# Kernel optimization log

Hardware: AMD Instinct MI355X
Metric: run time of the kernel (lower is better)

The kernel has to match this reference:

```python
import jax, jax.numpy as jnp
import numpy as np

N_NODES = 1111
BRANCH = 10


def _build_parents(n, b):
    parents = np.zeros(n, dtype=np.int32)
    for i in range(1, n):
        parents[i] = (i - 1) // b
    return parents


def _levels_from_parents(parents):
    n = parents.shape[0]
    depth = np.zeros(n, dtype=np.int32)
    for i in range(1, n):
        depth[i] = depth[parents[i]] + 1
    return [np.nonzero(depth == d)[0] for d in range(int(depth.max()) + 1)]


def setup_inputs() -> dict:
    key = jax.random.key(0)
    ks = jax.random.split(key, 8)
    N, B, Din, M = N_NODES, 128, 300, 256
    s = 0.05
    parents = _build_parents(N, BRANCH)
    return {
        "inputs": jax.random.normal(ks[0], (N, B, Din), jnp.float32),
        "prob": jax.random.uniform(ks[1], (N, N), jnp.float32),
        "Wioux": jax.random.normal(ks[2], (3 * M, Din), jnp.float32) * s,
        "bioux": jnp.zeros((3 * M,), jnp.float32),
        "Wiouh": jax.random.normal(ks[3], (3 * M, M), jnp.float32) * s,
        "biouh": jnp.zeros((3 * M,), jnp.float32),
        "Wfx": jax.random.normal(ks[4], (M, Din), jnp.float32) * s,
        "bfx": jnp.zeros((M,), jnp.float32),
        "Wfh": jax.random.normal(ks[5], (M, M), jnp.float32) * s,
        "bfh": jnp.zeros((M,), jnp.float32),
        "parents": jnp.asarray(parents),
    }


def reference(inputs, prob, Wioux, bioux, Wiouh, biouh, Wfx, bfx, Wfh, bfh, parents):
    # inputs: [N, B, Din]; prob: [N, N]; Linear weights in torch layout [out, in].
    N, B, _ = inputs.shape
    M = Wfx.shape[0]
    parents_np = np.asarray(parents)
    levels = _levels_from_parents(parents_np)  # static tree structure

    # Input-dependent pre-activations for all nodes at once (batched over the tree).
    xiou = jnp.einsum('nbd,kd->nbk', inputs, Wioux) + bioux  # [N, B, 3M]
    xf = jnp.einsum('nbd,md->nbm', inputs, Wfx) + bfx        # [N, B, M]

    h = jnp.zeros((N, B, M), inputs.dtype)
    c = jnp.zeros((N, B, M), inputs.dtype)

    # Level-synchronous top-down pass: all nodes at a given depth share no
    # dependencies, so each level is one batched gating step (loop over ~4 levels).
    for d, idx in enumerate(levels):
        if d == 0:
            ph = jnp.zeros((len(idx), B, M), inputs.dtype)
            pc = ph
        else:
            p = parents_np[idx]
            scale = prob[p, idx][:, None, None]  # edge weight prob[parent, child]
            ph = scale * h[p]
            pc = scale * c[p]
        iou = xiou[idx] + jnp.einsum('nbm,km->nbk', ph, Wiouh) + biouh
        i, o, u = jnp.split(iou, 3, axis=-1)
        f = jax.nn.sigmoid(jnp.einsum('nbm,km->nbk', ph, Wfh) + bfh + xf[idx])
        cn = jax.nn.sigmoid(i) * jnp.tanh(u) + f * pc
        hn = jax.nn.sigmoid(o) * jnp.tanh(cn)
        c = c.at[idx].set(cn)
        h = h.at[idx].set(hn)

    # Per-node top_down_state for the whole tree (original stores these on nodes
    # and returns the root's (c, h)).
    return c, h
```

## Files before the change

kernel.cpp:

```cpp
#include <hip/hip_runtime.h>
#include <hip/hip_bf16.h>


#define NNODES 1111
#define BATCH  128
#define MDIM   256
#define DIN    300
#define NBM    (NNODES * BATCH * MDIM)
#define NCK_X  10
#define NCK_H  8
#define CHUNK_ELEMS 8192
#define XW_ELEMS (4 * NCK_X * CHUNK_ELEMS)
#define HW_ELEMS (4 * NCK_H * CHUNK_ELEMS)

typedef __attribute__((ext_vector_type(8))) short s16x8;
typedef __attribute__((ext_vector_type(4))) float f32x4;

__device__ __forceinline__ ushort f2bf(float f) {
    union { float f; unsigned u; } v; v.f = f;
    unsigned u = v.u;
    return (ushort)((u + 0x7FFFu + ((u >> 16) & 1u)) >> 16);
}
__device__ __forceinline__ float bf2f(ushort u) {
    union { unsigned u; float f; } v; v.u = ((unsigned)u) << 16;
    return v.f;
}
__device__ __forceinline__ float sigmoidf_(float x) { return 1.0f / (1.0f + __expf(-x)); }

__device__ __forceinline__ int swz(int a) { return a ^ (((a >> 6) & 7) << 4); }

__global__ void prep_kernel(
    const float* __restrict__ Wioux, const float* __restrict__ bioux,
    const float* __restrict__ Wiouh, const float* __restrict__ biouh,
    const float* __restrict__ Wfx,   const float* __restrict__ bfx,
    const float* __restrict__ Wfh,   const float* __restrict__ bfh,
    ushort* __restrict__ packWx, ushort* __restrict__ packWh,
    float* __restrict__ bias)
{
    const int idx = blockIdx.x * 256 + threadIdx.x;
    if (idx < XW_ELEMS + HW_ELEMS) {
        const bool isX = idx < XW_ELEMS;
        const int id   = isX ? idx : idx - XW_ELEMS;
        const int nck  = isX ? NCK_X : NCK_H;
        const int strip = id / (nck * CHUNK_ELEMS);
        const int rem   = id % (nck * CHUNK_ELEMS);
        const int ck    = rem / CHUNK_ELEMS;
        const int e     = rem % CHUNK_ELEMS;
        const int pb  = e * 2;
        const int grp = pb >> 9;
        const int low = pb & 511;
        const int b4 = (low >> 4) & 1, b5 = (low >> 5) & 1, b6 = (low >> 6) & 1;
        const int b7 = (low >> 7) & 1, b8 = (low >> 8) & 1;
        const int a6 = b6 ^ b8, a5 = b5 ^ b7, a4 = b4 ^ a6;
        const int a = (grp << 9) | (low & 15) | (a4 << 4) | (a5 << 5) | (a6 << 6) | (b7 << 7) | (b8 << 8);
        const int lrow = a >> 6;
        const int kl   = (a & 63) >> 1;
        const int g = lrow >> 6, rowin = lrow & 63;
        const int j = g * 256 + strip * 64 + rowin;
        const int k = ck * 32 + kl;
        float val = 0.0f;
        if (isX) {
            if (k < DIN) val = (j < 768) ? Wioux[j * DIN + k] : Wfx[(j - 768) * DIN + k];
            packWx[id] = f2bf(val);
        } else {
            val = (j < 768) ? Wiouh[j * MDIM + k] : Wfh[(j - 768) * MDIM + k];
            packWh[id] = f2bf(val);
        }
    } else if (idx < XW_ELEMS + HW_ELEMS + 1024) {
        const int b = idx - XW_ELEMS - HW_ELEMS;
        bias[b] = (b < 768) ? (bioux[b] + biouh[b]) : (bfx[b - 768] + bfh[b - 768]);
    }
}

template<int MODE>
__global__ __launch_bounds__(512, 4) void level_kernel(
    const float* __restrict__ Asrc,
    const float* __restrict__ prob,
    const ushort* __restrict__ packW,
    const float* __restrict__ bias,
    float* __restrict__ out,
    ushort* __restrict__ HF,
    int level_start, int plevel_start)
{
    constexpr int NCK = (MODE == 2) ? NCK_H : NCK_X;
    constexpr int AST = (MODE == 2) ? MDIM : DIN;

    __shared__ __align__(16) ushort ldsA[2][BATCH * 32];
    __shared__ __align__(16) ushort ldsW[2][256 * 32];

    const int tid   = threadIdx.x;
    const int node  = level_start + (blockIdx.x >> 2);
    const int strip = blockIdx.x & 3;
    const int c0    = strip * 64;

    int parent = 0; float scale = 0.0f;
    if (MODE == 1) {
        parent = (node - 1) / 10;
        scale  = prob[(size_t)parent * NNODES + node];
    }

    const int wave = tid >> 6, lane = tid & 63;
    const int wr = wave >> 2, wm = wave & 3;
    const int l15 = lane & 15, kq = lane >> 4;

    f32x4 acc[4][4];
    const f32x4 zero4 = {0.f, 0.f, 0.f, 0.f};
#pragma unroll
    for (int t = 0; t < 4; ++t)
#pragma unroll
        for (int g = 0; g < 4; ++g) acc[t][g] = zero4;

    const int srow = tid >> 2;
    const int se8  = (tid & 3) * 8;
    const float* arow = Asrc + ((size_t)node * BATCH + srow) * AST;
    const int aOff = swz(srow * 64 + se8 * 2);

    int aoff[4], boff[4];
#pragma unroll
    for (int t = 0; t < 4; ++t) aoff[t] = swz((wr * 64 + t * 16 + l15) * 64 + kq * 16);
#pragma unroll
    for (int g = 0; g < 4; ++g) boff[g] = swz((g * 64 + wm * 16 + l15) * 64 + kq * 16);

    const ushort* wbase = packW + (size_t)(strip * NCK) * CHUNK_ELEMS;

    float4 va0, va1;
    auto issueA = [&](int ck) {
        const float* p = arow + ck * 32 + se8;
        va0 = *(const float4*)p;
        va1 = *(const float4*)(p + 4);
    };
    auto writeA = [&](int ck, int buf) {
        float v[8] = {va0.x, va0.y, va0.z, va0.w, va1.x, va1.y, va1.z, va1.w};
        if (MODE != 2) {
            const int ge = ck * 32 + se8;
            if (ge + 7 >= DIN) {
#pragma unroll
                for (int j = 0; j < 8; ++j) if (ge + j >= DIN) v[j] = 0.0f;
            }
        }
        union { ushort us[8]; int4 q; } pk;
#pragma unroll
        for (int j = 0; j < 8; ++j) pk.us[j] = f2bf(v[j]);
        *(int4*)((char*)ldsA[buf] + aOff) = pk.q;
    };
    auto issueW = [&](int ck, int buf) {
        const ushort* g0 = wbase + (size_t)ck * CHUNK_ELEMS + wave * 1024 + lane * 8;
        ushort* l0 = &ldsW[buf][wave * 1024];
        __builtin_amdgcn_global_load_lds(
            (const __attribute__((address_space(1))) unsigned*)(const void*)g0,
            (__attribute__((address_space(3))) unsigned*)(void*)l0, 16, 0, 0);
        __builtin_amdgcn_global_load_lds(
            (const __attribute__((address_space(1))) unsigned*)(const void*)(g0 + 512),
            (__attribute__((address_space(3))) unsigned*)(void*)(l0 + 512), 16, 0, 0);
    };

    issueA(0);
    issueW(0, 0);
    writeA(0, 0);
    asm volatile("s_waitcnt vmcnt(0) lgkmcnt(0)" ::: "memory");
    __builtin_amdgcn_sched_barrier(0);
    __builtin_amdgcn_s_barrier();
    __builtin_amdgcn_sched_barrier(0);

    int cur = 0;
    for (int t = 0; t < NCK - 1; ++t) {
        issueA(t + 1);
        issueW(t + 1, cur ^ 1);
        s16x8 af[4], bfr[4];
        char* pA = (char*)ldsA[cur];
        char* pW = (char*)ldsW[cur];
#pragma unroll
        for (int i = 0; i < 4; ++i) af[i] = *(const s16x8*)(pA + aoff[i]);
#pragma unroll
        for (int g = 0; g < 4; ++g) bfr[g] = *(const s16x8*)(pW + boff[g]);
#pragma unroll
        for (int i = 0; i < 4; ++i)
#pragma unroll
            for (int g = 0; g < 4; ++g)
                acc[i][g] = __builtin_amdgcn_mfma_f32_16x16x32_bf16(af[i], bfr[g], acc[i][g], 0, 0, 0);
        writeA(t + 1, cur ^ 1);
        asm volatile("s_waitcnt vmcnt(0) lgkmcnt(0)" ::: "memory");
        __builtin_amdgcn_sched_barrier(0);
        __builtin_amdgcn_s_barrier();
        __builtin_amdgcn_sched_barrier(0);
        cur ^= 1;
    }
    {
        s16x8 af[4], bfr[4];
        char* pA = (char*)ldsA[cur];
        char* pW = (char*)ldsW[cur];
#pragma unroll
        for (int i = 0; i < 4; ++i) af[i] = *(const s16x8*)(pA + aoff[i]);
#pragma unroll
        for (int g = 0; g < 4; ++g) bfr[g] = *(const s16x8*)(pW + boff[g]);
#pragma unroll
        for (int i = 0; i < 4; ++i)
#pragma unroll
            for (int g = 0; g < 4; ++g)
                acc[i][g] = __builtin_amdgcn_mfma_f32_16x16x32_bf16(af[i], bfr[g], acc[i][g], 0, 0, 0);
    }

    const int m = c0 + wm * 16 + l15;

    if (MODE == 2) {
        ushort* hfw = HF + (size_t)(node - level_start) * BATCH * 1024;
#pragma unroll
        for (int t = 0; t < 4; ++t) {
            const int b0 = wr * 64 + t * 16 + (kq << 2);
#pragma unroll
            for (int r = 0; r < 4; ++r) {
                const int brow = b0 + r;
#pragma unroll
                for (int g = 0; g < 4; ++g)
                    hfw[(size_t)brow * 1024 + g * 256 + m] = f2bf(acc[t][g][r]);
            }
        }
        return;
    }

    const float bi  = bias[m];
    const float bo  = bias[256 + m];
    const float bu  = bias[512 + m];
    const float bfv = bias[768 + m];
    const float* cprev = out + (size_t)parent * BATCH * MDIM;
    const ushort* hfb = (MODE == 1) ? (HF + (size_t)(parent - plevel_start) * BATCH * 1024) : (const ushort*)0;
    float* cOut = out;
    float* hOut = out + NBM;

#pragma unroll
    for (int t = 0; t < 4; ++t) {
        const int b0 = wr * 64 + t * 16 + (kq << 2);
#pragma unroll
        for (int r = 0; r < 4; ++r) {
            const int brow = b0 + r;
            float hi = 0.f, ho = 0.f, hu = 0.f, hff = 0.f, pc = 0.f;
            if (MODE == 1) {
                const ushort* hr = hfb + (size_t)brow * 1024;
                hi  = bf2f(hr[m]);
                ho  = bf2f(hr[256 + m]);
                hu  = bf2f(hr[512 + m]);
                hff = bf2f(hr[768 + m]);
                pc  = scale * cprev[(size_t)brow * MDIM + m];
            }
            const float iv = acc[t][0][r] + bi  + scale * hi;
            const float ov = acc[t][1][r] + bo  + scale * ho;
            const float uv = acc[t][2][r] + bu  + scale * hu;
            const float fv = acc[t][3][r] + bfv + scale * hff;
            const float cn = sigmoidf_(iv) * tanhf(uv) + sigmoidf_(fv) * pc;
            const float hn = sigmoidf_(ov) * tanhf(cn);
            const size_t o = ((size_t)node * BATCH + brow) * MDIM + m;
            cOut[o] = cn;
            hOut[o] = hn;
        }
    }
}

extern "C" void kernel_launch(void* const* d_in, const int* in_sizes, int n_in,
                              void* d_out, int out_size, void* d_ws, size_t ws_size,
                              hipStream_t stream) {
    const float* inputs = (const float*)d_in[0];
    const float* prob   = (const float*)d_in[1];
    const float* Wioux  = (const float*)d_in[2];
    const float* bioux  = (const float*)d_in[3];
    const float* Wiouh  = (const float*)d_in[4];
    const float* biouh  = (const float*)d_in[5];
    const float* Wfx    = (const float*)d_in[6];
    const float* bfx    = (const float*)d_in[7];
    const float* Wfh    = (const float*)d_in[8];
    const float* bfh    = (const float*)d_in[9];
    float* out = (float*)d_out;

    ushort* packWx = (ushort*)d_ws;
    ushort* packWh = packWx + XW_ELEMS;
    float*  bias   = (float*)(packWh + HW_ELEMS);
    ushort* HF     = (ushort*)(bias + 1024);

    const int prepTotal = XW_ELEMS + HW_ELEMS + 1024;
    prep_kernel<<<(prepTotal + 255) / 256, 256, 0, stream>>>(
        Wioux, bioux, Wiouh, biouh, Wfx, bfx, Wfh, bfh, packWx, packWh, bias);

    const float* hsec = out + NBM;

    level_kernel<0><<<dim3(4),    512, 0, stream>>>(inputs, prob, packWx, bias, out, HF, 0, 0);
    level_kernel<2><<<dim3(4),    512, 0, stream>>>(hsec,   prob, packWh, bias, out, HF, 0, 0);
    level_kernel<1><<<dim3(40),   512, 0, stream>>>(inputs, prob, packWx, bias, out, HF, 1, 0);
    level_kernel<2><<<dim3(40),   512, 0, stream>>>(hsec,   prob, packWh, bias, out, HF, 1, 1);
    level_kernel<1><<<dim3(400),  512, 0, stream>>>(inputs, prob, packWx, bias, out, HF, 11, 1);
    level_kernel<2><<<dim3(400),  512, 0, stream>>>(hsec,   prob, packWh, bias, out, HF, 11, 11);
    level_kernel<1><<<dim3(4000), 512, 0, stream>>>(inputs, prob, packWx, bias, out, HF, 111, 11);
}
```

Measured before the change: 739.9 us.

## Fold bias into padded K column, fast gates, vectorized HF layout, relaxed waits

Bias is folded into the x-weight pack at padded column 319, with the matching A element set to 1.0, so the separate bias loads and adds go away. Sigmoid and tanh now use hardware reciprocal plus exp approximations. The HF intermediate moves to an MFMA-fragment-native layout so writes and reads become vectorized per-thread accesses. The pipeline now waits only for the previous chunk's loads before computing (vmcnt(4)) and converts to bf16 with packed intrinsics. Risks are lower accuracy in tanh/sigmoid and a bias rounded to bf16.

Result: faster. 704.9 us (-4.7%).

```diff
diff --git a/kernel.cpp b/kernel.cpp
--- a/kernel.cpp
+++ b/kernel.cpp
@@ -12,9 +12,12 @@
 #define CHUNK_ELEMS 8192
 #define XW_ELEMS (4 * NCK_X * CHUNK_ELEMS)
 #define HW_ELEMS (4 * NCK_H * CHUNK_ELEMS)
+#define HF_PER_PS 32768
+#define HF_PER_P  131072
 
 typedef __attribute__((ext_vector_type(8))) short s16x8;
 typedef __attribute__((ext_vector_type(4))) float f32x4;
+typedef __attribute__((ext_vector_type(4))) unsigned short u16x4;
 
 __device__ __forceinline__ ushort f2bf(float f) {
     union { float f; unsigned u; } v; v.f = f;
@@ -25,7 +28,12 @@
     union { unsigned u; float f; } v; v.u = ((unsigned)u) << 16;
     return v.f;
 }
-__device__ __forceinline__ float sigmoidf_(float x) { return 1.0f / (1.0f + __expf(-x)); }
+__device__ __forceinline__ float sig_(float x) {
+    return __builtin_amdgcn_rcpf(1.0f + __expf(-x));
+}
+__device__ __forceinline__ float tanh_(float x) {
+    return __builtin_fmaf(-2.0f, __builtin_amdgcn_rcpf(__expf(2.0f * x) + 1.0f), 1.0f);
+}
 
 __device__ __forceinline__ int swz(int a) { return a ^ (((a >> 6) & 7) << 4); }
 
@@ -34,41 +42,38 @@
     const float* __restrict__ Wiouh, const float* __restrict__ biouh,
     const float* __restrict__ Wfx,   const float* __restrict__ bfx,
     const float* __restrict__ Wfh,   const float* __restrict__ bfh,
-    ushort* __restrict__ packWx, ushort* __restrict__ packWh,
-    float* __restrict__ bias)
+    ushort* __restrict__ packWx, ushort* __restrict__ packWh)
 {
     const int idx = blockIdx.x * 256 + threadIdx.x;
-    if (idx < XW_ELEMS + HW_ELEMS) {
-        const bool isX = idx < XW_ELEMS;
-        const int id   = isX ? idx : idx - XW_ELEMS;
-        const int nck  = isX ? NCK_X : NCK_H;
-        const int strip = id / (nck * CHUNK_ELEMS);
-        const int rem   = id % (nck * CHUNK_ELEMS);
-        const int ck    = rem / CHUNK_ELEMS;
-        const int e     = rem % CHUNK_ELEMS;
-        const int pb  = e * 2;
-        const int grp = pb >> 9;
-        const int low = pb & 511;
-        const int b4 = (low >> 4) & 1, b5 = (low >> 5) & 1, b6 = (low >> 6) & 1;
-        const int b7 = (low >> 7) & 1, b8 = (low >> 8) & 1;
-        const int a6 = b6 ^ b8, a5 = b5 ^ b7, a4 = b4 ^ a6;
-        const int a = (grp << 9) | (low & 15) | (a4 << 4) | (a5 << 5) | (a6 << 6) | (b7 << 7) | (b8 << 8);
-        const int lrow = a >> 6;
-        const int kl   = (a & 63) >> 1;
-        const int g = lrow >> 6, rowin = lrow & 63;
-        const int j = g * 256 + strip * 64 + rowin;
-        const int k = ck * 32 + kl;
-        float val = 0.0f;
-        if (isX) {
-            if (k < DIN) val = (j < 768) ? Wioux[j * DIN + k] : Wfx[(j - 768) * DIN + k];
-            packWx[id] = f2bf(val);
-        } else {
-            val = (j < 768) ? Wiouh[j * MDIM + k] : Wfh[(j - 768) * MDIM + k];
-            packWh[id] = f2bf(val);
-        }
-    } else if (idx < XW_ELEMS + HW_ELEMS + 1024) {
-        const int b = idx - XW_ELEMS - HW_ELEMS;
-        bias[b] = (b < 768) ? (bioux[b] + biouh[b]) : (bfx[b - 768] + bfh[b - 768]);
+    if (idx >= XW_ELEMS + HW_ELEMS) return;
+    const bool isX = idx < XW_ELEMS;
+    const int id   = isX ? idx : idx - XW_ELEMS;
+    const int nck  = isX ? NCK_X : NCK_H;
+    const int strip = id / (nck * CHUNK_ELEMS);
+    const int rem   = id % (nck * CHUNK_ELEMS);
+    const int ck    = rem / CHUNK_ELEMS;
+    const int e     = rem % CHUNK_ELEMS;
+    const int pb  = e * 2;
+    const int grp = pb >> 9;
+    const int low = pb & 511;
+    const int b4 = (low >> 4) & 1, b5 = (low >> 5) & 1, b6 = (low >> 6) & 1;
+    const int b7 = (low >> 7) & 1, b8 = (low >> 8) & 1;
+    const int a6 = b6 ^ b8, a5 = b5 ^ b7, a4 = b4 ^ a6;
+    const int a = (grp << 9) | (low & 15) | (a4 << 4) | (a5 << 5) | (a6 << 6) | (b7 << 7) | (b8 << 8);
+    const int lrow = a >> 6;
+    const int kl   = (a & 63) >> 1;
+    const int g = lrow >> 6, rowin = lrow & 63;
+    const int j = g * 256 + strip * 64 + rowin;
+    const int k = ck * 32 + kl;
+    if (isX) {
+        float val;
+        if (k < DIN)       val = (j < 768) ? Wioux[j * DIN + k] : Wfx[(j - 768) * DIN + k];
+        else if (k == 319) val = (j < 768) ? (bioux[j] + biouh[j]) : (bfx[j - 768] + bfh[j - 768]);
+        else               val = 0.0f;
+        packWx[id] = f2bf(val);
+    } else {
+        const float val = (j < 768) ? Wiouh[j * MDIM + k] : Wfh[(j - 768) * MDIM + k];
+        packWh[id] = f2bf(val);
     }
 }
 
@@ -77,7 +82,6 @@
     const float* __restrict__ Asrc,
     const float* __restrict__ prob,
     const ushort* __restrict__ packW,
-    const float* __restrict__ bias,
     float* __restrict__ out,
     ushort* __restrict__ HF,
     int level_start, int plevel_start)
@@ -135,12 +139,16 @@
             const int ge = ck * 32 + se8;
             if (ge + 7 >= DIN) {
 #pragma unroll
-                for (int j = 0; j < 8; ++j) if (ge + j >= DIN) v[j] = 0.0f;
+                for (int j = 0; j < 8; ++j) {
+                    const int gk = ge + j;
+                    if (gk >= DIN) v[j] = (gk == 319) ? 1.0f : 0.0f;
+                }
             }
         }
-        union { ushort us[8]; int4 q; } pk;
-#pragma unroll
-        for (int j = 0; j < 8; ++j) pk.us[j] = f2bf(v[j]);
+        union { __hip_bfloat162 h2[4]; int4 q; } pk;
+#pragma unroll
+        for (int j = 0; j < 4; ++j)
+            pk.h2[j] = __float22bfloat162_rn(make_float2(v[2 * j], v[2 * j + 1]));
         *(int4*)((char*)ldsA[buf] + aOff) = pk.q;
     };
     auto issueW = [&](int ck, int buf) {
@@ -153,101 +161,96 @@
             (const __attribute__((address_space(1))) unsigned*)(const void*)(g0 + 512),
             (__attribute__((address_space(3))) unsigned*)(void*)(l0 + 512), 16, 0, 0);
     };
+    auto compute = [&](int buf) {
+        s16x8 af[4], bfr[4];
+        char* pA = (char*)ldsA[buf];
+        char* pW = (char*)ldsW[buf];
+#pragma unroll
+        for (int i = 0; i < 4; ++i) af[i] = *(const s16x8*)(pA + aoff[i]);
+#pragma unroll
+        for (int g = 0; g < 4; ++g) bfr[g] = *(const s16x8*)(pW + boff[g]);
+#pragma unroll
+        for (int i = 0; i < 4; ++i)
+#pragma unroll
+            for (int g = 0; g < 4; ++g)
+                acc[i][g] = __builtin_amdgcn_mfma_f32_16x16x32_bf16(af[i], bfr[g], acc[i][g], 0, 0, 0);
+    };
 
     issueA(0);
     issueW(0, 0);
     writeA(0, 0);
+
+    int b = 0;
+    for (int t = 0; t < NCK - 1; ++t) {
+        issueA(t + 1);
+        issueW(t + 1, b ^ 1);
+        asm volatile("s_waitcnt vmcnt(4) lgkmcnt(0)" ::: "memory");
+        __builtin_amdgcn_sched_barrier(0);
+        __builtin_amdgcn_s_barrier();
+        __builtin_amdgcn_sched_barrier(0);
+        compute(b);
+        writeA(t + 1, b ^ 1);
+        asm volatile("s_waitcnt lgkmcnt(0)" ::: "memory");
+        __builtin_amdgcn_sched_barrier(0);
+        __builtin_amdgcn_s_barrier();
+        __builtin_amdgcn_sched_barrier(0);
+        b ^= 1;
+    }
     asm volatile("s_waitcnt vmcnt(0) lgkmcnt(0)" ::: "memory");
     __builtin_amdgcn_sched_barrier(0);
     __builtin_amdgcn_s_barrier();
     __builtin_amdgcn_sched_barrier(0);
-
-    int cur = 0;
-    for (int t = 0; t < NCK - 1; ++t) {
-        issueA(t + 1);
-        issueW(t + 1, cur ^ 1);
-        s16x8 af[4], bfr[4];
-        char* pA = (char*)ldsA[cur];
-        char* pW = (char*)ldsW[cur];
-#pragma unroll
-        for (int i = 0; i < 4; ++i) af[i] = *(const s16x8*)(pA + aoff[i]);
-#pragma unroll
-        for (int g = 0; g < 4; ++g) bfr[g] = *(const s16x8*)(pW + boff[g]);
-#pragma unroll
-        for (int i = 0; i < 4; ++i)
-#pragma unroll
-            for (int g = 0; g < 4; ++g)
-                acc[i][g] = __builtin_amdgcn_mfma_f32_16x16x32_bf16(af[i], bfr[g], acc[i][g], 0, 0, 0);
-        writeA(t + 1, cur ^ 1);
-        asm volatile("s_waitcnt vmcnt(0) lgkmcnt(0)" ::: "memory");
-        __builtin_amdgcn_sched_barrier(0);
-        __builtin_amdgcn_s_barrier();
-        __builtin_amdgcn_sched_barrier(0);
-        cur ^= 1;
-    }
-    {
-        s16x8 af[4], bfr[4];
-        char* pA = (char*)ldsA[cur];
-        char* pW = (char*)ldsW[cur];
-#pragma unroll
-        for (int i = 0; i < 4; ++i) af[i] = *(const s16x8*)(pA + aoff[i]);
-#pragma unroll
-        for (int g = 0; g < 4; ++g) bfr[g] = *(const s16x8*)(pW + boff[g]);
-#pragma unroll
-        for (int i = 0; i < 4; ++i)
-#pragma unroll
-            for (int g = 0; g < 4; ++g)
-                acc[i][g] = __builtin_amdgcn_mfma_f32_16x16x32_bf16(af[i], bfr[g], acc[i][g], 0, 0, 0);
-    }
+    compute(b);
 
     const int m = c0 + wm * 16 + l15;
 
     if (MODE == 2) {
-        ushort* hfw = HF + (size_t)(node - level_start) * BATCH * 1024;
-#pragma unroll
-        for (int t = 0; t < 4; ++t) {
-            const int b0 = wr * 64 + t * 16 + (kq << 2);
-#pragma unroll
-            for (int r = 0; r < 4; ++r) {
-                const int brow = b0 + r;
-#pragma unroll
-                for (int g = 0; g < 4; ++g)
-                    hfw[(size_t)brow * 1024 + g * 256 + m] = f2bf(acc[t][g][r]);
+        ushort* hfw = HF + (size_t)(node - level_start) * HF_PER_P + strip * HF_PER_PS;
+#pragma unroll
+        for (int t = 0; t < 4; ++t)
+#pragma unroll
+            for (int g = 0; g < 4; ++g) {
+                union { __hip_bfloat162 h2[2]; uint2 q; } pk;
+                pk.h2[0] = __float22bfloat162_rn(make_float2(acc[t][g][0], acc[t][g][1]));
+                pk.h2[1] = __float22bfloat162_rn(make_float2(acc[t][g][2], acc[t][g][3]));
+                *(uint2*)(hfw + (t * 4 + g) * 2048 + tid * 4) = pk.q;
             }
-        }
         return;
     }
 
-    const float bi  = bias[m];
-    const float bo  = bias[256 + m];
-    const float bu  = bias[512 + m];
-    const float bfv = bias[768 + m];
     const float* cprev = out + (size_t)parent * BATCH * MDIM;
-    const ushort* hfb = (MODE == 1) ? (HF + (size_t)(parent - plevel_start) * BATCH * 1024) : (const ushort*)0;
+    const ushort* hfb = (MODE == 1)
+        ? (HF + (size_t)(parent - plevel_start) * HF_PER_P + strip * HF_PER_PS)
+        : (const ushort*)0;
     float* cOut = out;
     float* hOut = out + NBM;
 
 #pragma unroll
     for (int t = 0; t < 4; ++t) {
         const int b0 = wr * 64 + t * 16 + (kq << 2);
+        u16x4 qi = {0,0,0,0}, qo = {0,0,0,0}, qu = {0,0,0,0}, qf = {0,0,0,0};
+        if (MODE == 1) {
+            qi = *(const u16x4*)(hfb + (t * 4 + 0) * 2048 + tid * 4);
+            qo = *(const u16x4*)(hfb + (t * 4 + 1) * 2048 + tid * 4);
+            qu = *(const u16x4*)(hfb + (t * 4 + 2) * 2048 + tid * 4);
+            qf = *(const u16x4*)(hfb + (t * 4 + 3) * 2048 + tid * 4);
+        }
 #pragma unroll
         for (int r = 0; r < 4; ++r) {
             const int brow = b0 + r;
-            float hi = 0.f, ho = 0.f, hu = 0.f, hff = 0.f, pc = 0.f;
+            float cn, hn;
             if (MODE == 1) {
-                const ushort* hr = hfb + (size_t)brow * 1024;
-                hi  = bf2f(hr[m]);
-                ho  = bf2f(hr[256 + m]);
-                hu  = bf2f(hr[512 + m]);
-                hff = bf2f(hr[768 + m]);
-                pc  = scale * cprev[(size_t)brow * MDIM + m];
+                const float pc = scale * cprev[(size_t)brow * MDIM + m];
+                const float iv = __builtin_fmaf(scale, bf2f(qi[r]), acc[t][0][r]);
+                const float ov = __builtin_fmaf(scale, bf2f(qo[r]), acc[t][1][r]);
+                const float uv = __builtin_fmaf(scale, bf2f(qu[r]), acc[t][2][r]);
+                const float fv = __builtin_fmaf(scale, bf2f(qf[r]), acc[t][3][r]);
+                cn = sig_(iv) * tanh_(uv) + sig_(fv) * pc;
+                hn = sig_(ov) * tanh_(cn);
+            } else {
+                cn = sig_(acc[t][0][r]) * tanh_(acc[t][2][r]);
+                hn = sig_(acc[t][1][r]) * tanh_(cn);
             }
-            const float iv = acc[t][0][r] + bi  + scale * hi;
-            const float ov = acc[t][1][r] + bo  + scale * ho;
-            const float uv = acc[t][2][r] + bu  + scale * hu;
-            const float fv = acc[t][3][r] + bfv + scale * hff;
-            const float cn = sigmoidf_(iv) * tanhf(uv) + sigmoidf_(fv) * pc;
-            const float hn = sigmoidf_(ov) * tanhf(cn);
             const size_t o = ((size_t)node * BATCH + brow) * MDIM + m;
             cOut[o] = cn;
             hOut[o] = hn;
@@ -272,20 +275,19 @@
 
     ushort* packWx = (ushort*)d_ws;
     ushort* packWh = packWx + XW_ELEMS;
-    float*  bias   = (float*)(packWh + HW_ELEMS);
-    ushort* HF     = (ushort*)(bias + 1024);
-
-    const int prepTotal = XW_ELEMS + HW_ELEMS + 1024;
+    ushort* HF     = packWh + HW_ELEMS;
+
+    const int prepTotal = XW_ELEMS + HW_ELEMS;
     prep_kernel<<<(prepTotal + 255) / 256, 256, 0, stream>>>(
-        Wioux, bioux, Wiouh, biouh, Wfx, bfx, Wfh, bfh, packWx, packWh, bias);
+        Wioux, bioux, Wiouh, biouh, Wfx, bfx, Wfh, bfh, packWx, packWh);
 
     const float* hsec = out + NBM;
 
-    level_kernel<0><<<dim3(4),    512, 0, stream>>>(inputs, prob, packWx, bias, out, HF, 0, 0);
-    level_kernel<2><<<dim3(4),    512, 0, stream>>>(hsec,   prob, packWh, bias, out, HF, 0, 0);
-    level_kernel<1><<<dim3(40),   512, 0, stream>>>(inputs, prob, packWx, bias, out, HF, 1, 0);
-    level_kernel<2><<<dim3(40),   512, 0, stream>>>(hsec,   prob, packWh, bias, out, HF, 1, 1);
-    level_kernel<1><<<dim3(400),  512, 0, stream>>>(inputs, prob, packWx, bias, out, HF, 11, 1);
-    level_kernel<2><<<dim3(400),  512, 0, stream>>>(hsec,   prob, packWh, bias, out, HF, 11, 11);
-    level_kernel<1><<<dim3(4000), 512, 0, stream>>>(inputs, prob, packWx, bias, out, HF, 111, 11);
-}
+    level_kernel<0><<<dim3(4),    512, 0, stream>>>(inputs, prob, packWx, out, HF, 0, 0);
+    level_kernel<2><<<dim3(4),    512, 0, stream>>>(hsec,   prob, packWh, out, HF, 0, 0);
+    level_kernel<1><<<dim3(40),   512, 0, stream>>>(inputs, prob, packWx, out, HF, 1, 0);
+    level_kernel<2><<<dim3(40),   512, 0, stream>>>(hsec,   prob, packWh, out, HF, 1, 1);
+    level_kernel<1><<<dim3(400),  512, 0, stream>>>(inputs, prob, packWx, out, HF, 11, 1);
+    level_kernel<2><<<dim3(400),  512, 0, stream>>>(hsec,   prob, packWh, out, HF, 11, 11);
+    level_kernel<1><<<dim3(4000), 512, 0, stream>>>(inputs, prob, packWx, out, HF, 111, 11);
+}
```
